# Optimization experiments

Hardware: AMD Instinct MI355X
Metric: run time of the kernel (lower is better)

Reference implementation:

```python
import jax, jax.numpy as jnp
import numpy as np

H = 6        # attn heads (hardcoded in DinoPool forward via view(..., 6, 64))
D = 64       # head dim
BLOCK = 512  # block-diagonal mask window (stands in for the torch BlockMask)


def setup_inputs() -> dict:
    key = jax.random.key(0)
    k1, k2, k3 = jax.random.split(key, 3)
    B, S = 4, 4096
    x = jax.random.normal(k1, (B, S, H * D), dtype=jnp.float32)
    x1 = jax.random.normal(k2, (B, S, H * D), dtype=jnp.float32)  # unused by module
    x2 = jax.random.normal(k3, (B, S, H * D), dtype=jnp.float32)  # unused by module
    # block-diagonal mask: q attends to kv within the same BLOCK-sized window
    blk = jnp.arange(S) // BLOCK
    mask = blk[:, None] == blk[None, :]  # [S, S] bool
    return {"x": x, "x1": x1, "x2": x2, "mask": mask}


def reference(x, x1, x2, mask):
    # score_mod returns score*0+1: all unmasked scores are equal, so softmax is a
    # uniform average over unmasked kv positions -> masked average pooling over V.
    B, S, _ = x.shape
    v = x.reshape(B, S, H, D).transpose(0, 2, 1, 3)          # [B, H, S, D]
    m = mask.astype(x.dtype)                                  # [S, S]
    denom = m.sum(axis=-1)                                    # [S], count of unmasked kv per q
    numer = jnp.einsum('qk,bhkd->bhqd', m, v)                 # masked sum over kv
    y = numer / denom[None, None, :, None]                    # [B, H, S, D]
    return y.transpose(0, 2, 1, 3).reshape(B, S, H * D)       # [B, S, H*D]
```

## Files before the change

kernel.cpp:

```cpp
#include <hip/hip_runtime.h>


#define BB   4
#define SS   4096
#define CC   384
#define BLK  512
#define NBLK 8
#define NT   384
#define NSUB 16
#define RWS  (BLK / NSUB)

__global__ __launch_bounds__(NT) void colsum_f32(
    const float* __restrict__ x, float* __restrict__ ws, int rch) {
  int bid = blockIdx.x;
  int r   = bid % rch;
  int blk = (bid / rch) % NBLK;
  int b   = bid / (rch * NBLK);
  int c   = threadIdx.x;
  int rows = BLK / rch;

  const float* p = x + (size_t)(b * SS + blk * BLK + r * rows) * CC + c;
  float acc = 0.0f;
#pragma unroll 16
  for (int i = 0; i < rows; ++i) acc += p[(size_t)i * CC];
  ws[(size_t)bid * CC + c] = acc;
}

__global__ __launch_bounds__(NT) void bcast_f32(
    const float* __restrict__ ws, float* __restrict__ out, int rch) {
  __shared__ __align__(16) float smean[CC];

  int bid = blockIdx.x;
  int sub = bid & (NSUB - 1);
  int blk = (bid >> 4) & (NBLK - 1);
  int b   = bid >> 7;
  int t   = threadIdx.x;

  const float* wp = ws + (size_t)((b * NBLK + blk) * rch) * CC + t;
  float s = 0.0f;
  for (int r = 0; r < rch; ++r) s += wp[(size_t)r * CC];
  smean[t] = s * (1.0f / (float)BLK);
  __syncthreads();

  const float4* sv = (const float4*)smean;
  float4* ov = (float4*)(out + (size_t)(b * SS + blk * BLK + sub * RWS) * CC);
  const int total = RWS * (CC / 4);
  for (int i = t; i < total; i += NT) ov[i] = sv[i % 96];
}

__global__ __launch_bounds__(NT) void fused_f32(
    const float* __restrict__ x, float* __restrict__ out) {
  __shared__ float part[4][CC];
  __shared__ __align__(16) float smean[CC];

  int bid = blockIdx.x;
  int sub = bid & (NSUB - 1);
  int blk = (bid >> 4) & (NBLK - 1);
  int b   = bid >> 7;
  int t   = threadIdx.x;
  int cq  = t % 96;
  int g   = t / 96;

  const float4* xv = (const float4*)(x + (size_t)(b * SS + blk * BLK) * CC);
  float a0 = 0.f, a1 = 0.f, a2 = 0.f, a3 = 0.f;
  for (int k = 0; k < BLK / 4; ++k) {
    float4 v = xv[(size_t)(g + 4 * k) * 96 + cq];
    a0 += v.x; a1 += v.y; a2 += v.z; a3 += v.w;
  }
  part[g][cq * 4 + 0] = a0;
  part[g][cq * 4 + 1] = a1;
  part[g][cq * 4 + 2] = a2;
  part[g][cq * 4 + 3] = a3;
  __syncthreads();

  float s = 0.f;
#pragma unroll
  for (int gg = 0; gg < 4; ++gg) s += part[gg][t];
  smean[t] = s * (1.0f / (float)BLK);
  __syncthreads();

  const float4* sv = (const float4*)smean;
  float4* ov = (float4*)(out + (size_t)(b * SS + blk * BLK + sub * RWS) * CC);
  const int total = RWS * (CC / 4);
  for (int i = t; i < total; i += NT) ov[i] = sv[i % 96];
}

extern "C" void kernel_launch(void* const* d_in, const int* in_sizes, int n_in,
                              void* d_out, int out_size, void* d_ws,
                              size_t ws_size, hipStream_t stream) {
  const float* x = (const float*)d_in[0];
  float* out = (float*)d_out;
  float* ws = (float*)d_ws;

  const size_t per_rch = (size_t)BB * NBLK * CC * sizeof(float);
  int rch = 0;
  if (ws_size >= 8 * per_rch)      rch = 8;
  else if (ws_size >= 4 * per_rch) rch = 4;
  else if (ws_size >= 2 * per_rch) rch = 2;
  else if (ws_size >= 1 * per_rch) rch = 1;

  if (rch > 0) {
    colsum_f32<<<BB * NBLK * rch, NT, 0, stream>>>(x, ws, rch);
    bcast_f32<<<BB * NBLK * NSUB, NT, 0, stream>>>(ws, out, rch);
  } else {
    fused_f32<<<BB * NBLK * NSUB, NT, 0, stream>>>(x, out);
  }
}
```

Before: 143.8 us.

## Fuse column-sum and broadcast into one cooperative kernel with grid sync

Replaces the two-kernel column-sum then broadcast pipeline with a single cooperative-launch kernel. Each of 256 workgroups sums its slice of rows, writes a partial to workspace, waits at a grid-wide barrier, then reduces the partials and writes the mean to its own rows. This removes a kernel launch boundary but limits the grid to 256 workgroups for the write phase and adds grid-sync cost. It falls back to the two-kernel path if the cooperative launch fails, and it drops the workspace-size check and the fused fallback kernel.

```diff
diff --git a/kernel.cpp b/kernel.cpp
--- a/kernel.cpp
+++ b/kernel.cpp
@@ -1,4 +1,7 @@
 #include <hip/hip_runtime.h>
+#include <hip/hip_cooperative_groups.h>
+
+namespace cg = cooperative_groups;
 
 
 #define BB   4
@@ -7,81 +10,71 @@
 #define BLK  512
 #define NBLK 8
 #define NT   384
-#define NSUB 16
-#define RWS  (BLK / NSUB)
+#define RCH  8
+#define ROWS (BLK / RCH)
+
+__global__ __launch_bounds__(NT) void dinopool_coop(
+    const float* __restrict__ x, float* __restrict__ ws,
+    float* __restrict__ out) {
+  int bid = blockIdx.x;
+  int r   = bid & (RCH - 1);
+  int blk = (bid >> 3) & (NBLK - 1);
+  int b   = bid >> 6;
+  int t   = threadIdx.x;
+
+  const float* p = x + (size_t)(b * SS + blk * BLK + r * ROWS) * CC + t;
+  float acc = 0.0f;
+#pragma unroll 16
+  for (int i = 0; i < ROWS; ++i) acc += p[(size_t)i * CC];
+  ws[(size_t)bid * CC + t] = acc;
+
+  cg::this_grid().sync();
+
+  __shared__ __align__(16) float smean[CC];
+  const float* wp = ws + (size_t)((b * NBLK + blk) * RCH) * CC + t;
+  float s = 0.0f;
+#pragma unroll
+  for (int k = 0; k < RCH; ++k) s += wp[(size_t)k * CC];
+  smean[t] = s * (1.0f / (float)BLK);
+  __syncthreads();
+
+  const float4* sv = (const float4*)smean;
+  float4* ov = (float4*)(out + (size_t)(b * SS + blk * BLK + r * ROWS) * CC);
+  const int total = ROWS * (CC / 4);
+  for (int i = t; i < total; i += NT) ov[i] = sv[i % 96];
+}
 
 __global__ __launch_bounds__(NT) void colsum_f32(
-    const float* __restrict__ x, float* __restrict__ ws, int rch) {
+    const float* __restrict__ x, float* __restrict__ ws) {
   int bid = blockIdx.x;
-  int r   = bid % rch;
-  int blk = (bid / rch) % NBLK;
-  int b   = bid / (rch * NBLK);
+  int r   = bid & (RCH - 1);
+  int blk = (bid >> 3) & (NBLK - 1);
+  int b   = bid >> 6;
   int c   = threadIdx.x;
-  int rows = BLK / rch;
-
-  const float* p = x + (size_t)(b * SS + blk * BLK + r * rows) * CC + c;
+  const float* p = x + (size_t)(b * SS + blk * BLK + r * ROWS) * CC + c;
   float acc = 0.0f;
 #pragma unroll 16
-  for (int i = 0; i < rows; ++i) acc += p[(size_t)i * CC];
+  for (int i = 0; i < ROWS; ++i) acc += p[(size_t)i * CC];
   ws[(size_t)bid * CC + c] = acc;
 }
 
 __global__ __launch_bounds__(NT) void bcast_f32(
-    const float* __restrict__ ws, float* __restrict__ out, int rch) {
+    const float* __restrict__ ws, float* __restrict__ out) {
   __shared__ __align__(16) float smean[CC];
-
   int bid = blockIdx.x;
-  int sub = bid & (NSUB - 1);
+  int sub = bid & 15;
   int blk = (bid >> 4) & (NBLK - 1);
   int b   = bid >> 7;
   int t   = threadIdx.x;
-
-  const float* wp = ws + (size_t)((b * NBLK + blk) * rch) * CC + t;
+  const float* wp = ws + (size_t)((b * NBLK + blk) * RCH) * CC + t;
   float s = 0.0f;
-  for (int r = 0; r < rch; ++r) s += wp[(size_t)r * CC];
+#pragma unroll
+  for (int k = 0; k < RCH; ++k) s += wp[(size_t)k * CC];
   smean[t] = s * (1.0f / (float)BLK);
   __syncthreads();
-
   const float4* sv = (const float4*)smean;
-  float4* ov = (float4*)(out + (size_t)(b * SS + blk * BLK + sub * RWS) * CC);
-  const int total = RWS * (CC / 4);
-  for (int i = t; i < total; i += NT) ov[i] = sv[i % 96];
-}
-
-__global__ __launch_bounds__(NT) void fused_f32(
-    const float* __restrict__ x, float* __restrict__ out) {
-  __shared__ float part[4][CC];
-  __shared__ __align__(16) float smean[CC];
-
-  int bid = blockIdx.x;
-  int sub = bid & (NSUB - 1);
-  int blk = (bid >> 4) & (NBLK - 1);
-  int b   = bid >> 7;
-  int t   = threadIdx.x;
-  int cq  = t % 96;
-  int g   = t / 96;
-
-  const float4* xv = (const float4*)(x + (size_t)(b * SS + blk * BLK) * CC);
-  float a0 = 0.f, a1 = 0.f, a2 = 0.f, a3 = 0.f;
-  for (int k = 0; k < BLK / 4; ++k) {
-    float4 v = xv[(size_t)(g + 4 * k) * 96 + cq];
-    a0 += v.x; a1 += v.y; a2 += v.z; a3 += v.w;
-  }
-  part[g][cq * 4 + 0] = a0;
-  part[g][cq * 4 + 1] = a1;
-  part[g][cq * 4 + 2] = a2;
-  part[g][cq * 4 + 3] = a3;
-  __syncthreads();
-
-  float s = 0.f;
-#pragma unroll
-  for (int gg = 0; gg < 4; ++gg) s += part[gg][t];
-  smean[t] = s * (1.0f / (float)BLK);
-  __syncthreads();
-
-  const float4* sv = (const float4*)smean;
-  float4* ov = (float4*)(out + (size_t)(b * SS + blk * BLK + sub * RWS) * CC);
-  const int total = RWS * (CC / 4);
+  float4* ov = (float4*)(out + (size_t)(b * SS + blk * BLK + sub * 32) * CC);
+  const int total = 32 * (CC / 4);
   for (int i = t; i < total; i += NT) ov[i] = sv[i % 96];
 }
 
@@ -92,17 +85,12 @@
   float* out = (float*)d_out;
   float* ws = (float*)d_ws;
 
-  const size_t per_rch = (size_t)BB * NBLK * CC * sizeof(float);
-  int rch = 0;
-  if (ws_size >= 8 * per_rch)      rch = 8;
-  else if (ws_size >= 4 * per_rch) rch = 4;
-  else if (ws_size >= 2 * per_rch) rch = 2;
-  else if (ws_size >= 1 * per_rch) rch = 1;
-
-  if (rch > 0) {
-    colsum_f32<<<BB * NBLK * rch, NT, 0, stream>>>(x, ws, rch);
-    bcast_f32<<<BB * NBLK * NSUB, NT, 0, stream>>>(ws, out, rch);
-  } else {
-    fused_f32<<<BB * NBLK * NSUB, NT, 0, stream>>>(x, out);
+  void* args[] = {(void*)&x, (void*)&ws, (void*)&out};
+  hipError_t err = hipLaunchCooperativeKernel(
+      (const void*)dinopool_coop, dim3(BB * NBLK * RCH), dim3(NT), args, 0,
+      stream);
+  if (err != hipSuccess) {
+    colsum_f32<<<BB * NBLK * RCH, NT, 0, stream>>>(x, ws);
+    bcast_f32<<<BB * NBLK * 16, NT, 0, stream>>>(ws, out);
   }
 }
```

After: 179.1 us. 24.6% more time.

## Replace two-pass colsum/broadcast with single fused kernel and interleaved block order

Applied to the files above, without the earlier changes.

Removes the workspace-based column-sum plus broadcast kernels and always launches one fused kernel where every output block recomputes its window's column mean. Block indices are remapped so the sub-blocks sharing one window are spread across concurrent groups, aiming to serve the redundant input reads from cache. This saves a kernel launch and the workspace round trip, at the cost of reading each input window sixteen times.

```diff
diff --git a/kernel.cpp b/kernel.cpp
--- a/kernel.cpp
+++ b/kernel.cpp
@@ -9,62 +9,27 @@
 #define NT   384
 #define NSUB 16
 #define RWS  (BLK / NSUB)
+#define CH4  (CC / 4)
 
-__global__ __launch_bounds__(NT) void colsum_f32(
-    const float* __restrict__ x, float* __restrict__ ws, int rch) {
-  int bid = blockIdx.x;
-  int r   = bid % rch;
-  int blk = (bid / rch) % NBLK;
-  int b   = bid / (rch * NBLK);
-  int c   = threadIdx.x;
-  int rows = BLK / rch;
-
-  const float* p = x + (size_t)(b * SS + blk * BLK + r * rows) * CC + c;
-  float acc = 0.0f;
-#pragma unroll 16
-  for (int i = 0; i < rows; ++i) acc += p[(size_t)i * CC];
-  ws[(size_t)bid * CC + c] = acc;
-}
-
-__global__ __launch_bounds__(NT) void bcast_f32(
-    const float* __restrict__ ws, float* __restrict__ out, int rch) {
-  __shared__ __align__(16) float smean[CC];
-
-  int bid = blockIdx.x;
-  int sub = bid & (NSUB - 1);
-  int blk = (bid >> 4) & (NBLK - 1);
-  int b   = bid >> 7;
-  int t   = threadIdx.x;
-
-  const float* wp = ws + (size_t)((b * NBLK + blk) * rch) * CC + t;
-  float s = 0.0f;
-  for (int r = 0; r < rch; ++r) s += wp[(size_t)r * CC];
-  smean[t] = s * (1.0f / (float)BLK);
-  __syncthreads();
-
-  const float4* sv = (const float4*)smean;
-  float4* ov = (float4*)(out + (size_t)(b * SS + blk * BLK + sub * RWS) * CC);
-  const int total = RWS * (CC / 4);
-  for (int i = t; i < total; i += NT) ov[i] = sv[i % 96];
-}
-
-__global__ __launch_bounds__(NT) void fused_f32(
+__global__ __launch_bounds__(NT) void dinopool_fused(
     const float* __restrict__ x, float* __restrict__ out) {
   __shared__ float part[4][CC];
   __shared__ __align__(16) float smean[CC];
 
-  int bid = blockIdx.x;
-  int sub = bid & (NSUB - 1);
-  int blk = (bid >> 4) & (NBLK - 1);
-  int b   = bid >> 7;
-  int t   = threadIdx.x;
-  int cq  = t % 96;
-  int g   = t / 96;
+  int bid   = blockIdx.x;
+  int group = bid & 31;
+  int sub   = bid >> 5;
+  int blk   = group & (NBLK - 1);
+  int b     = group >> 3;
+  int t     = threadIdx.x;
+  int cq    = t % CH4;
+  int g     = t / CH4;
 
   const float4* xv = (const float4*)(x + (size_t)(b * SS + blk * BLK) * CC);
   float a0 = 0.f, a1 = 0.f, a2 = 0.f, a3 = 0.f;
+#pragma unroll 8
   for (int k = 0; k < BLK / 4; ++k) {
-    float4 v = xv[(size_t)(g + 4 * k) * 96 + cq];
+    float4 v = xv[(size_t)(g + 4 * k) * CH4 + cq];
     a0 += v.x; a1 += v.y; a2 += v.z; a3 += v.w;
   }
   part[g][cq * 4 + 0] = a0;
@@ -81,8 +46,8 @@
 
   const float4* sv = (const float4*)smean;
   float4* ov = (float4*)(out + (size_t)(b * SS + blk * BLK + sub * RWS) * CC);
-  const int total = RWS * (CC / 4);
-  for (int i = t; i < total; i += NT) ov[i] = sv[i % 96];
+  const int total = RWS * CH4;
+  for (int i = t; i < total; i += NT) ov[i] = sv[i % CH4];
 }
 
 extern "C" void kernel_launch(void* const* d_in, const int* in_sizes, int n_in,
@@ -90,19 +55,5 @@
                               size_t ws_size, hipStream_t stream) {
   const float* x = (const float*)d_in[0];
   float* out = (float*)d_out;
-  float* ws = (float*)d_ws;
-
-  const size_t per_rch = (size_t)BB * NBLK * CC * sizeof(float);
-  int rch = 0;
-  if (ws_size >= 8 * per_rch)      rch = 8;
-  else if (ws_size >= 4 * per_rch) rch = 4;
-  else if (ws_size >= 2 * per_rch) rch = 2;
-  else if (ws_size >= 1 * per_rch) rch = 1;
-
-  if (rch > 0) {
-    colsum_f32<<<BB * NBLK * rch, NT, 0, stream>>>(x, ws, rch);
-    bcast_f32<<<BB * NBLK * NSUB, NT, 0, stream>>>(ws, out, rch);
-  } else {
-    fused_f32<<<BB * NBLK * NSUB, NT, 0, stream>>>(x, out);
-  }
+  dinopool_fused<<<BB * NBLK * NSUB, NT, 0, stream>>>(x, out);
 }
```

New measurement: 153.0 us. +6.4%, slower.
